# Optimization experiments

Measured on AMD Instinct MI355X. Metric: run time of the kernel, lower is better.

Reference implementation:

```python
import jax, jax.numpy as jnp
import numpy as np

# Fixed production-scale dims (see shape_source)
B, R, WIDTH, T, H, W = 8, 12, 2304, 4, 16, 29
REDUCE, HID, NC, ROI_SP, DEPTH = 1024, 512, 60, 7, 2
SR = 2  # roi_align sampling ratio (fixed; torchvision default -1 is roi-adaptive)


def conv2d(x, w, pad):
    return jax.lax.conv_general_dilated(
        x, w, (1, 1), [(pad, pad), (pad, pad)],
        dimension_numbers=('NCHW', 'OIHW', 'NCHW'))


def maxpool_3x3_s2(x):
    return jax.lax.reduce_window(
        x, -jnp.inf, jax.lax.max, (1, 1, 3, 3), (1, 1, 2, 2),
        [(0, 0), (0, 0), (1, 1), (1, 1)])


def bilinear(img, ys, xs):
    # img [C,h,w]; ys, xs [P] -> [C,P]; matches torchvision bilinear_interpolate
    h, w = img.shape[1], img.shape[2]
    valid = (ys >= -1.0) & (ys <= h) & (xs >= -1.0) & (xs <= w)
    y = jnp.clip(ys, 0.0, h - 1.0)
    x = jnp.clip(xs, 0.0, w - 1.0)
    y0f = jnp.floor(y); x0f = jnp.floor(x)
    iy0 = y0f.astype(jnp.int32); ix0 = x0f.astype(jnp.int32)
    iy1 = jnp.minimum(iy0 + 1, h - 1); ix1 = jnp.minimum(ix0 + 1, w - 1)
    ly = y - y0f; lx = x - x0f; hy = 1.0 - ly; hx = 1.0 - lx
    v00 = img[:, iy0, ix0]; v01 = img[:, iy0, ix1]
    v10 = img[:, iy1, ix0]; v11 = img[:, iy1, ix1]
    out = hy * hx * v00 + hy * lx * v01 + ly * hx * v10 + ly * lx * v11
    return jnp.where(valid[None, :], out, 0.0)


def roi_align_one(img, box):
    # img [C,H,W]; box (x1,y1,x2,y2) in feature coords; aligned=False, scale=1
    x1, y1, x2, y2 = box[0], box[1], box[2], box[3]
    rw = jnp.maximum(x2 - x1, 1.0)
    rh = jnp.maximum(y2 - y1, 1.0)
    bw = rw / ROI_SP; bh = rh / ROI_SP
    g = (jnp.arange(ROI_SP, dtype=jnp.float32)[:, None]
         + (jnp.arange(SR, dtype=jnp.float32)[None, :] + 0.5) / SR).reshape(-1)  # [7*SR]
    ys = y1 + g * bh; xs = x1 + g * bw
    n = ROI_SP * SR
    yy = jnp.repeat(ys, n); xx = jnp.tile(xs, n)
    vals = bilinear(img, yy, xx)                       # [C, n*n]
    vals = vals.reshape(img.shape[0], ROI_SP, SR, ROI_SP, SR)
    return vals.mean(axis=(2, 4))                      # [C,7,7]


def hr2o_layer(x, qw, kw, vw, cw, gamma, beta):
    # x [R, HID, Hp, Wp]; non-local attention across ROIs of one image
    q = conv2d(x, qw, 1)
    k = conv2d(x, kw, 1)
    v = conv2d(x, vw, 1)
    att = jnp.einsum('ichw,jchw->ijhw', q, k) / jnp.sqrt(jnp.float32(HID))
    att = jax.nn.softmax(att, axis=1)                  # softmax over key rois
    virt = jnp.einsum('ijhw,jchw->ichw', att, v)
    mu = virt.mean(axis=(1, 2, 3), keepdims=True)      # GroupNorm(1, HID)
    var = virt.var(axis=(1, 2, 3), keepdims=True)
    virt = (virt - mu) / jnp.sqrt(var + 1e-5)
    virt = virt * gamma[None, :, None, None] + beta[None, :, None, None]
    virt = jax.nn.relu(virt)
    virt = conv2d(virt, cw, 1)                         # mlp_1x1=False -> 3x3 pad 1
    return x + virt                                    # dropout inactive in eval


def setup_inputs() -> dict:
    key = jax.random.key(0)
    ks = jax.random.split(key, 14)
    features = jax.random.normal(ks[0], (B, WIDTH, T, H, W), jnp.float32)
    xy = jax.random.uniform(ks[1], (B, R, 2), minval=0.0, maxval=0.6)
    wh = jax.random.uniform(ks[2], (B, R, 2), minval=0.2, maxval=0.4)
    rois = jnp.concatenate([xy, xy + wh], axis=-1)     # normalized x1,y1,x2,y2

    def w_(k, shape, fan_in):
        return jax.random.normal(k, shape, jnp.float32) * (1.0 / np.sqrt(fan_in))

    return {
        'features': features,
        'rois': rois,
        'conv_reduce_w': w_(ks[3], (REDUCE, WIDTH, 1, 1), WIDTH),
        'conv1_w': w_(ks[4], (HID, 2 * REDUCE, 1, 1), 2 * REDUCE),
        'conv2_w': w_(ks[5], (HID, HID, 3, 3), HID * 9),
        'hr2o_qw': w_(ks[6], (DEPTH, HID, HID, 3, 3), HID * 9),
        'hr2o_kw': w_(ks[7], (DEPTH, HID, HID, 3, 3), HID * 9),
        'hr2o_vw': w_(ks[8], (DEPTH, HID, HID, 3, 3), HID * 9),
        'hr2o_cw': w_(ks[9], (DEPTH, HID, HID, 3, 3), HID * 9),
        'hr2o_gamma': jnp.ones((DEPTH, HID), jnp.float32),
        'hr2o_beta': jnp.zeros((DEPTH, HID), jnp.float32),
        'fc1_w': w_(ks[10], (HID, REDUCE), REDUCE),
        'fc2_w': w_(ks[11], (NC, 2 * HID), 2 * HID),
    }


def reference(features, rois, conv_reduce_w, conv1_w, conv2_w,
              hr2o_qw, hr2o_kw, hr2o_vw, hr2o_cw, hr2o_gamma, hr2o_beta,
              fc1_w, fc2_w):
    feats = features.mean(axis=2)                      # AdaptiveAvgPool3d((1,H,W)) over T
    feats = conv2d(feats, conv_reduce_w, 0)            # [B, REDUCE, H, W]

    scale = jnp.array([W, H, W, H], jnp.float32)
    boxes = rois * scale                               # feature-space coords (detached)
    ra = jax.vmap(lambda img, bxs: jax.vmap(lambda b: roi_align_one(img, b))(bxs))(
        feats, boxes)                                  # [B, R, REDUCE, 7, 7]
    roi_feats = ra.max(axis=(-2, -1)).reshape(B * R, REDUCE)  # MaxPool2d(7)

    # broadcast bg + tiled actor, concat on channels (eff_h=H, eff_w=W)
    bg = jnp.broadcast_to(feats[:, None], (B, R, REDUCE, H, W))
    actor = jnp.broadcast_to(
        roi_feats.reshape(B, R, REDUCE)[..., None, None], (B, R, REDUCE, H, W))
    x = jnp.concatenate([bg, actor], axis=2).reshape(B * R, 2 * REDUCE, H, W)
    x = jax.nn.relu(conv2d(x, conv1_w, 0))             # 1x1
    x = jax.nn.relu(conv2d(x, conv2_w, 0))             # 3x3, Conv2d default pad=0
    x = maxpool_3x3_s2(x)                              # [B*R, HID, 7, 14]
    hp, wp = x.shape[2], x.shape[3]
    x = x.reshape(B, R, HID, hp, wp)
    for d in range(DEPTH):
        x = jax.vmap(lambda xi: hr2o_layer(
            xi, hr2o_qw[d], hr2o_kw[d], hr2o_vw[d], hr2o_cw[d],
            hr2o_gamma[d], hr2o_beta[d]))(x)
    high = x.mean(axis=(-2, -1)).reshape(B * R, HID)   # GAP

    out = jax.nn.relu(roi_feats @ fc1_w.T)
    out = jnp.concatenate([out, high], axis=1)
    return out @ fc2_w.T                               # [B*R, NC]
```

## Files before the change

### kernel.cpp

```cpp
#include <hip/hip_runtime.h>
#include <math.h>

#define BB 8
#define RR 12
#define WIDTH 2304
#define TT 4
#define HH 16
#define WW 29
#define HWIN (HH*WW)
#define REDUCE 1024
#define HID 512
#define NC 60
#define DEPTH 2
#define NIMG (BB*RR)
#define OH2 14
#define OW2 27
#define NSP2 (OH2*OW2)
#define PH 7
#define PW 14
#define NSP (PH*PW)
#define ATT_SCALE 0.044194173824159216f

typedef __attribute__((ext_vector_type(8))) short short8;
typedef __attribute__((ext_vector_type(4))) float floatx4;

__device__ __forceinline__ void split2(float v, unsigned short& h, unsigned short& l)
{
    union { float f; unsigned u; } c; c.f = v;
    unsigned hb = c.u & 0xffff0000u;
    h = (unsigned short)(hb >> 16);
    union { float f; unsigned u; } hc; hc.u = hb;
    float r = v - hc.f;
    union { float f; unsigned u; } rc; rc.f = r;
    unsigned ru = rc.u + 0x7fffu + ((rc.u >> 16) & 1u);
    l = (unsigned short)(ru >> 16);
}

__device__ __forceinline__ void gll16(const void* g, void* l)
{
    __builtin_amdgcn_global_load_lds((const __attribute__((address_space(1))) void*)g,
                                     (__attribute__((address_space(3))) void*)l,
                                     16, 0, 0);
}

#define MFMA3(d, ah_, al_, bh_, bl_) \
    d = __builtin_amdgcn_mfma_f32_16x16x32_bf16(ah_, bh_, d, 0, 0, 0); \
    d = __builtin_amdgcn_mfma_f32_16x16x32_bf16(ah_, bl_, d, 0, 0, 0); \
    d = __builtin_amdgcn_mfma_f32_16x16x32_bf16(al_, bh_, d, 0, 0, 0);

template<int TYPE, int NSEL, bool RELU, bool RESID, int KW, int KSTN, int MTOT, long PLSTR, int NREAL>
__global__ __launch_bounds__(256, 2)
void tap2_k(const int4* __restrict__ WA0, const int4* __restrict__ WA1, const int4* __restrict__ WA2,
            const ushort* __restrict__ BH, const ushort* __restrict__ BL,
            const float* __restrict__ Res,
            float* __restrict__ Y0, float* __restrict__ Y1, float* __restrict__ Y2)
{
    __shared__ int4 L[3872];
    const int tid = threadIdx.x;
    const int z = blockIdx.z, nb = blockIdx.x;
    int by = blockIdx.y;

    const int4* WA = WA0; float* Y = Y0;
    if (NSEL == 3) {
        int sel = by >> 2; by &= 3;
        if (sel == 1) { WA = WA1; Y = Y1; }
        else if (sel == 2) { WA = WA2; Y = Y2; }
    }
    const int m0 = by * 128;
    const int lane = tid & 63, wv = tid >> 6;
    const int lrow = lane >> 4, lcol = lane & 15;
    constexpr long ALO = (long)KSTN * 4 * MTOT;

    int nU[2], gU[2]; long pbU[2]; bool vU[2];
#pragma unroll
    for (int it = 0; it < 2; ++it) {
        int u = tid + (it << 8);
        vU[it] = (u < 448);
        int uu = vU[it] ? u : 0;
        nU[it] = uu % 112; gU[it] = uu / 112;
        if (TYPE == 0) pbU[it] = nU[it];
        else {
            int gn = nb * 112 + nU[it];
            if (TYPE == 1) pbU[it] = (gn >> 5) * 29 + (gn & 31);
            else pbU[it] = min(gn, NREAL - 1);
        }
    }
    const ushort* BHz = BH + (size_t)z * PLSTR;
    const ushort* BLz = BL + (size_t)z * PLSTR;

    floatx4 acc[2][7];
#pragma unroll
    for (int mf = 0; mf < 2; ++mf)
#pragma unroll
        for (int nf = 0; nf < 7; ++nf) acc[mf][nf] = (floatx4){0.f, 0.f, 0.f, 0.f};

    short8 rbh[2], rbl[2];

#define STAGE_ISSUE(KST, BUF) { \
    int k8 = (KST) * 4; \
    _Pragma("unroll") \
    for (int j = 0; j < 4; ++j) { \
        int h = wv * 4 + j, p = h >> 3, g = (h >> 1) & 3, hf = h & 1; \
        gll16(WA + (p ? ALO : 0) + (long)(k8 + g) * MTOT + m0 + hf * 64 + lane, \
              L + (BUF) * 1936 + (p * 4 + g) * 129 + hf * 64); \
    } \
    int tap, ci0, shv; \
    if (TYPE == 2) { tap = 0; ci0 = (KST) << 5; shv = 0; } \
    else { tap = (KST) >> 4; ci0 = ((KST) & 15) << 5; int t3 = tap / 3; \
           shv = (TYPE == 0) ? t3 * 16 + (tap - t3 * 3) : t3 * 29 + (tap - t3 * 3); } \
    _Pragma("unroll") \
    for (int it = 0; it < 2; ++it) if (vU[it]) { \
        size_t o = (size_t)(pbU[it] + shv) * KW + ci0 + gU[it] * 8; \
        rbh[it] = *(const short8*)(BHz + o); \
        rbl[it] = *(const short8*)(BLz + o); \
    } }

#define STAGE_WRITE(BUF) { \
    _Pragma("unroll") \
    for (int it = 0; it < 2; ++it) if (vU[it]) { \
        *((short8*)(L + (BUF) * 1936 + 1032 + gU[it] * 113 + nU[it])) = rbh[it]; \
        *((short8*)(L + (BUF) * 1936 + 1484 + gU[it] * 113 + nU[it])) = rbl[it]; \
    } }

#define COMPUTE(BUF) { \
    const int4* Lc = L + (BUF) * 1936; \
    short8 ah[2], al[2]; \
    _Pragma("unroll") \
    for (int mf = 0; mf < 2; ++mf) { \
        int au = lrow * 129 + (wv * 2 + mf) * 16 + lcol; \
        ah[mf] = *(const short8*)(Lc + au); \
        al[mf] = *(const short8*)(Lc + 516 + au); \
    } \
    _Pragma("unroll") \
    for (int nf = 0; nf < 7; ++nf) { \
        int bu = 1032 + lrow * 113 + nf * 16 + lcol; \
        short8 bh = *(const short8*)(Lc + bu); \
        short8 bl = *(const short8*)(Lc + bu + 452); \
        _Pragma("unroll") \
        for (int mf = 0; mf < 2; ++mf) { MFMA3(acc[mf][nf], ah[mf], al[mf], bh, bl) } \
    } }

    STAGE_ISSUE(0, 0)
    STAGE_WRITE(0)
    __syncthreads();

    int cur = 0;
    for (int kst = 0; kst < KSTN; ++kst) {
        int nxt = cur ^ 1;
        bool more = (kst + 1 < KSTN);
        if (more) STAGE_ISSUE(kst + 1, nxt)
        COMPUTE(cur)
        if (more) { STAGE_WRITE(nxt) __syncthreads(); }
        cur = nxt;
    }

#pragma unroll
    for (int mf = 0; mf < 2; ++mf) {
        int m = m0 + wv * 32 + mf * 16 + lrow * 4;
#pragma unroll
        for (int nf = 0; nf < 7; ++nf) {
            int col = nf * 16 + lcol;
            int sp, realn; bool ok;
            if (TYPE == 0) { int oh = col >> 4, ow = col & 15; ok = ow < 14; sp = oh * 14 + ow; realn = 98; }
            else if (TYPE == 1) { int gn = nb * 112 + col; int oh = gn >> 5, ow = gn & 31; ok = ow < 27; sp = oh * 27 + ow; realn = 378; }
            else { int gn = nb * 112 + col; ok = gn < NREAL; sp = gn; realn = NREAL; }
            if (ok) {
#pragma unroll
                for (int r = 0; r < 4; ++r) {
                    size_t idx = ((size_t)z * MTOT + m + r) * realn + sp;
                    float v = acc[mf][nf][r];
                    if (RESID) v += Res[idx];
                    if (RELU) v = fmaxf(v, 0.f);
                    Y[idx] = v;
                }
            }
        }
    }
#undef STAGE_ISSUE
#undef STAGE_WRITE
#undef COMPUTE
}

__global__ void prep_w_k(const float* __restrict__ s0, const float* __restrict__ s1,
                         const float* __restrict__ s2, const float* __restrict__ s3,
                         int4* __restrict__ dst)
{
    const int c = blockIdx.y;
    const float* src = (c == 0) ? s0 : (c == 1) ? s1 : (c == 2) ? s2 : s3;
    int4* dh = dst + (size_t)c * 589824;
    int4* dl = dh + 294912;
    int idx = blockIdx.x * 256 + threadIdx.x;
    if (idx >= 294912) return;
    int g8 = idx / 512, m = idx & 511;
    unsigned hw[4], lw[4];
#pragma unroll
    for (int j = 0; j < 4; ++j) {
        int k1 = g8 * 8 + 2 * j, k2 = k1 + 1;
        float v1 = src[(size_t)m * 4608 + ((k1 & 511) * 9 + (k1 >> 9))];
        float v2 = src[(size_t)m * 4608 + ((k2 & 511) * 9 + (k2 >> 9))];
        unsigned short h0, l0, h1, l1;
        split2(v1, h0, l0); split2(v2, h1, l1);
        hw[j] = (unsigned)h0 | ((unsigned)h1 << 16);
        lw[j] = (unsigned)l0 | ((unsigned)l1 << 16);
    }
    dh[idx] = make_int4(hw[0], hw[1], hw[2], hw[3]);
    dl[idx] = make_int4(lw[0], lw[1], lw[2], lw[3]);
}

__global__ void prep_wg_k(const float* __restrict__ src, int ldw, int M, int K8,
                          int4* __restrict__ dst)
{
    int idx = blockIdx.x * 256 + threadIdx.x;
    if (idx >= K8 * M) return;
    int g8 = idx / M, m = idx % M;
    unsigned hw[4], lw[4];
#pragma unroll
    for (int j = 0; j < 4; ++j) {
        int k1 = g8 * 8 + 2 * j;
        float v1 = src[(size_t)m * ldw + k1];
        float v2 = src[(size_t)m * ldw + k1 + 1];
        unsigned short h0, l0, h1, l1;
        split2(v1, h0, l0); split2(v2, h1, l1);
        hw[j] = (unsigned)h0 | ((unsigned)h1 << 16);
        lw[j] = (unsigned)l0 | ((unsigned)l1 << 16);
    }
    dst[idx] = make_int4(hw[0], hw[1], hw[2], hw[3]);
    dst[(size_t)K8 * M + idx] = make_int4(lw[0], lw[1], lw[2], lw[3]);
}

__global__ __launch_bounds__(256)
void tsplit_k(const float* __restrict__ src, ushort* __restrict__ dh, ushort* __restrict__ dl,
              int C, int S, long zsrc, long zdst)
{
    __shared__ float t[64][65];
    const int c0 = blockIdx.x * 64, s0 = blockIdx.y * 64, z = blockIdx.z;
    const float* sz = src + (size_t)z * zsrc;
    const int tx = threadIdx.x & 63, ty = threadIdx.x >> 6;
#pragma unroll
    for (int i = 0; i < 16; ++i) {
        int cc = i * 4 + ty;
        int c = c0 + cc, s = s0 + tx;
        t[cc][tx] = (c < C && s < S) ? sz[(size_t)c * S + s] : 0.f;
    }
    __syncthreads();
#pragma unroll
    for (int i = 0; i < 16; ++i) {
        int ss = i * 4 + ty;
        int s = s0 + ss, c = c0 + tx;
        if (s < S && c < C) {
            unsigned short h, l;
            split2(t[tx][ss], h, l);
            size_t o = (size_t)z * zdst + (size_t)s * C + c;
            dh[o] = h; dl[o] = l;
        }
    }
}

__global__ __launch_bounds__(256)
void tsplit_c2_k(const float* __restrict__ bg, const float* __restrict__ bias1,
                 ushort* __restrict__ dh, ushort* __restrict__ dl)
{
    __shared__ float t[64][65];
    const int c0 = blockIdx.x * 64, s0 = blockIdx.y * 64, z = blockIdx.z;
    const int b = z / RR;
    const int tx = threadIdx.x & 63, ty = threadIdx.x >> 6;
#pragma unroll
    for (int i = 0; i < 16; ++i) {
        int cc = i * 4 + ty;
        int s = s0 + tx;
        t[cc][tx] = (s < 464) ? bg[((size_t)b * 512 + c0 + cc) * 464 + s] : 0.f;
    }
    __syncthreads();
    const float bv = bias1[z * 512 + c0 + tx];
#pragma unroll
    for (int i = 0; i < 16; ++i) {
        int ss = i * 4 + ty;
        int s = s0 + ss, c = c0 + tx;
        if (s < 472) {
            float v = (s < 464) ? fmaxf(t[tx][ss] + bv, 0.f) : 0.f;
            unsigned short h, l;
            split2(v, h, l);
            size_t o = (size_t)z * 241664 + (size_t)s * 512 + c;
            dh[o] = h; dl[o] = l;
        }
    }
}

__global__ __launch_bounds__(256)
void tsplit_pad_k(const float* __restrict__ x, ushort* __restrict__ dh, ushort* __restrict__ dl)
{
    __shared__ float t[64 * 99];
    const int c0 = blockIdx.x * 64, z = blockIdx.y;
    const int tid = threadIdx.x;
#pragma unroll
    for (int i = 0; i < 25; ++i) {
        int idx = tid + i * 256;
        if (idx < 6272) {
            int c = idx / 98, s = idx % 98;
            t[c * 99 + s] = x[((size_t)z * 512 + c0 + c) * 98 + s];
        }
    }
    __syncthreads();
#pragma unroll
    for (int i = 0; i < 40; ++i) {
        int idx = tid + i * 256;
        int sp = idx >> 6, c = idx & 63;
        int r = sp >> 4, col = sp & 15;
        float v = (r >= 1 && r <= 7 && col >= 1 && col <= 14) ? t[c * 99 + (r - 1) * 14 + col - 1] : 0.f;
        unsigned short h, l;
        split2(v, h, l);
        size_t o = (size_t)z * 81920 + (size_t)sp * 512 + c0 + c;
        dh[o] = h; dl[o] = l;
    }
}

__global__ void tmean_k(const float* __restrict__ f, float* __restrict__ o, int total)
{
    int i = blockIdx.x * blockDim.x + threadIdx.x;
    if (i >= total) return;
    int p = i % HWIN; long bc = i / HWIN;
    const float* src = f + bc * (long)TT * HWIN + p;
    o[i] = (src[0] + src[HWIN] + src[2 * HWIN] + src[3 * HWIN]) * 0.25f;
}

__global__ __launch_bounds__(256)
void roi_align_k(const float* __restrict__ feats, const float* __restrict__ rois,
                 float* __restrict__ roi_feats)
{
    __shared__ int s_o00[196], s_o01[196], s_o10[196], s_o11[196];
    __shared__ float s_w[4][196];
    const int n = blockIdx.x;
    const int b = n / RR;
    const int t = threadIdx.x;
    if (t < 196) {
        float x1 = rois[n * 4 + 0] * WW, y1 = rois[n * 4 + 1] * HH;
        float x2 = rois[n * 4 + 2] * WW, y2 = rois[n * 4 + 3] * HH;
        float rw = fmaxf(x2 - x1, 1.f), rh = fmaxf(y2 - y1, 1.f);
        float bw = rw / 7.f, bh = rh / 7.f;
        int j = t / 14, i = t % 14;
        float gy = (float)(j >> 1) + ((j & 1) + 0.5f) * 0.5f;
        float gx = (float)(i >> 1) + ((i & 1) + 0.5f) * 0.5f;
        float ys = y1 + gy * bh, xs = x1 + gx * bw;
        bool valid = (ys >= -1.f) && (ys <= (float)HH) && (xs >= -1.f) && (xs <= (float)WW);
        float y = fminf(fmaxf(ys, 0.f), (float)(HH - 1));
        float x = fminf(fmaxf(xs, 0.f), (float)(WW - 1));
        float y0f = floorf(y), x0f = floorf(x);
        int iy0 = (int)y0f, ix0 = (int)x0f;
        int iy1 = min(iy0 + 1, HH - 1), ix1 = min(ix0 + 1, WW - 1);
        float ly = y - y0f, lx = x - x0f, hy = 1.f - ly, hx = 1.f - lx;
        float msk = valid ? 1.f : 0.f;
        s_o00[t] = iy0 * WW + ix0; s_o01[t] = iy0 * WW + ix1;
        s_o10[t] = iy1 * WW + ix0; s_o11[t] = iy1 * WW + ix1;
        s_w[0][t] = hy * hx * msk; s_w[1][t] = hy * lx * msk;
        s_w[2][t] = ly * hx * msk; s_w[3][t] = ly * lx * msk;
    }
    __syncthreads();
    for (int c = t; c < REDUCE; c += 256) {
        const float* img = feats + ((long)(b * REDUCE + c)) * HWIN;
        float mx = -INFINITY;
        for (int bin = 0; bin < 49; ++bin) {
            int by_ = bin / 7, bx = bin % 7;
            float s = 0.f;
#pragma unroll
            for (int sy = 0; sy < 2; ++sy)
#pragma unroll
                for (int sx = 0; sx < 2; ++sx) {
                    int ss = (by_ * 2 + sy) * 14 + bx * 2 + sx;
                    s += s_w[0][ss] * img[s_o00[ss]] + s_w[1][ss] * img[s_o01[ss]]
                       + s_w[2][ss] * img[s_o10[ss]] + s_w[3][ss] * img[s_o11[ss]];
                }
            mx = fmaxf(mx, s * 0.25f);
        }
        roi_feats[(long)n * REDUCE + c] = mx;
    }
}

__global__ void dots_k(const float* __restrict__ Xr, const float* __restrict__ Wt,
                       int ldw, int woff, float* __restrict__ Y,
                       int Nrows, int M, int K, int relu)
{
    int idx = blockIdx.x * blockDim.x + threadIdx.x;
    if (idx >= Nrows * M) return;
    int o = idx / Nrows, n = idx % Nrows;
    const float* xr = Xr + (long)n * K;
    const float* w = Wt + (long)o * ldw + woff;
    float acc = 0.f;
    for (int k = 0; k < K; ++k) acc = fmaf(xr[k], w[k], acc);
    if (relu) acc = fmaxf(acc, 0.f);
    Y[(long)n * M + o] = acc;
}

__global__ void maxpool_k(const float* __restrict__ in, float* __restrict__ out, int total)
{
    int idx = blockIdx.x * blockDim.x + threadIdx.x;
    if (idx >= total) return;
    int ow = idx % PW; int r = idx / PW; int oh = r % PH; long nc = r / PH;
    const float* src = in + nc * NSP2;
    float m = -INFINITY;
    for (int kh = 0; kh < 3; ++kh) {
        int ih = oh * 2 - 1 + kh; if (ih < 0 || ih >= OH2) continue;
        for (int kw = 0; kw < 3; ++kw) {
            int iw = ow * 2 - 1 + kw; if (iw < 0 || iw >= OW2) continue;
            m = fmaxf(m, src[ih * OW2 + iw]);
        }
    }
    out[idx] = m;
}

__global__ void att_k(const float* __restrict__ q, const float* __restrict__ k,
                      float* __restrict__ att)
{
    int idx = blockIdx.x * blockDim.x + threadIdx.x;
    const int TOT = BB * 144 * 49;
    if (idx >= TOT) return;
    int ph = idx % 49; int r = idx / 49; int ij = r % 144; int b = r / 144;
    int i = ij / 12, j = ij % 12;
    int p = ph * 2;
    const float* qp = q + ((long)(b * RR + i) * HID) * NSP + p;
    const float* kp = k + ((long)(b * RR + j) * HID) * NSP + p;
    float a0 = 0.f, a1 = 0.f;
#pragma unroll 8
    for (int c = 0; c < HID; ++c) {
        float2 q2 = *(const float2*)(qp + (long)c * NSP);
        float2 k2 = *(const float2*)(kp + (long)c * NSP);
        a0 = fmaf(q2.x, k2.x, a0);
        a1 = fmaf(q2.y, k2.y, a1);
    }
    float* op = att + (((long)(b * 12 + i)) * 12 + j) * NSP + p;
    op[0] = a0 * ATT_SCALE;
    op[1] = a1 * ATT_SCALE;
}

__global__ void softmax_k(float* __restrict__ att)
{
    int idx = blockIdx.x * blockDim.x + threadIdx.x;
    const int TOT = BB * 12 * NSP;
    if (idx >= TOT) return;
    int p = idx % NSP; int r = idx / NSP; int i = r % 12; int b = r / 12;
    float* base = att + ((long)(b * 12 + i) * 12) * NSP + p;
    float v[12]; float m = -INFINITY;
#pragma unroll
    for (int j = 0; j < 12; ++j) { v[j] = base[j * NSP]; m = fmaxf(m, v[j]); }
    float s = 0.f;
#pragma unroll
    for (int j = 0; j < 12; ++j) { v[j] = expf(v[j] - m); s += v[j]; }
    float inv = 1.f / s;
#pragma unroll
    for (int j = 0; j < 12; ++j) base[j * NSP] = v[j] * inv;
}

__global__ void virt_k(const float* __restrict__ att, const float* __restrict__ v,
                       float* __restrict__ virt)
{
    int idx = blockIdx.x * blockDim.x + threadIdx.x;
    const int TOT = BB * RR * HID * 49;
    if (idx >= TOT) return;
    int ph = idx % 49; int r = idx / 49; int c = r % HID; int r2 = r / HID;
    int i = r2 % RR; int b = r2 / RR;
    int p = 2 * ph;
    const float* ap = att + ((long)(b * 12 + i) * 12) * NSP + p;
    float a0 = 0.f, a1 = 0.f;
#pragma unroll
    for (int j = 0; j < 12; ++j) {
        float w0 = ap[j * NSP], w1 = ap[j * NSP + 1];
        float2 v2 = *(const float2*)(v + (((long)(b * RR + j) * HID) + c) * NSP + p);
        a0 = fmaf(w0, v2.x, a0);
        a1 = fmaf(w1, v2.y, a1);
    }
    float* op = virt + (((long)(b * RR + i) * HID) + c) * NSP + p;
    op[0] = a0; op[1] = a1;
}

__global__ __launch_bounds__(256)
void stats_k(const float* __restrict__ virt, float* __restrict__ mu, float* __restrict__ rstd)
{
    int n = blockIdx.x;
    const float* src = virt + (long)n * HID * NSP;
    float s = 0.f, q = 0.f;
    for (int i = threadIdx.x; i < HID * NSP; i += 256) {
        float v = src[i]; s += v; q = fmaf(v, v, q);
    }
    for (int off = 32; off; off >>= 1) { s += __shfl_down(s, off); q += __shfl_down(q, off); }
    __shared__ float ss[4], sq[4];
    int w = threadIdx.x >> 6;
    if ((threadIdx.x & 63) == 0) { ss[w] = s; sq[w] = q; }
    __syncthreads();
    if (threadIdx.x == 0) {
        float S = ss[0] + ss[1] + ss[2] + ss[3];
        float Q = sq[0] + sq[1] + sq[2] + sq[3];
        const float invN = 1.f / (HID * NSP);
        float m = S * invN;
        float var = Q * invN - m * m;
        mu[n] = m; rstd[n] = rsqrtf(var + 1e-5f);
    }
}

__global__ void norm_k(float* __restrict__ virt, const float* __restrict__ mu,
                       const float* __restrict__ rstd,
                       const float* __restrict__ gamma, const float* __restrict__ beta)
{
    int idx = blockIdx.x * blockDim.x + threadIdx.x;
    const int TOT = NIMG * HID * NSP;
    if (idx >= TOT) return;
    int n = idx / (HID * NSP);
    int c = (idx / NSP) % HID;
    float val = (virt[idx] - mu[n]) * rstd[n] * gamma[c] + beta[c];
    virt[idx] = fmaxf(val, 0.f);
}

__global__ void meanpool_k(const float* __restrict__ x, float* __restrict__ high)
{
    int idx = blockIdx.x * blockDim.x + threadIdx.x;
    if (idx >= NIMG * HID) return;
    const float* src = x + (long)idx * NSP;
    float s = 0.f;
    for (int p = 0; p < NSP; ++p) s += src[p];
    high[idx] = s * (1.f / NSP);
}

__global__ void final_k(const float* __restrict__ fc1o, const float* __restrict__ high,
                        const float* __restrict__ fc2, float* __restrict__ out)
{
    int idx = blockIdx.x * blockDim.x + threadIdx.x;
    if (idx >= NIMG * NC) return;
    int n = idx / NC, o = idx % NC;
    const float* w = fc2 + (long)o * (2 * HID);
    const float* a = fc1o + (long)n * HID;
    const float* h = high + (long)n * HID;
    float acc = 0.f;
    for (int c = 0; c < HID; ++c) acc = fmaf(a[c], w[c], acc);
    for (int c = 0; c < HID; ++c) acc = fmaf(h[c], w[HID + c], acc);
    out[idx] = acc;
}

extern "C" void kernel_launch(void* const* d_in, const int* in_sizes, int n_in,
                              void* d_out, int out_size, void* d_ws, size_t ws_size,
                              hipStream_t stream)
{
    (void)in_sizes; (void)n_in; (void)out_size; (void)ws_size;
    const float* features = (const float*)d_in[0];
    const float* rois     = (const float*)d_in[1];
    const float* w_reduce = (const float*)d_in[2];
    const float* w_conv1  = (const float*)d_in[3];
    const float* w_conv2  = (const float*)d_in[4];
    const float* qw       = (const float*)d_in[5];
    const float* kw       = (const float*)d_in[6];
    const float* vw       = (const float*)d_in[7];
    const float* cw       = (const float*)d_in[8];
    const float* gamma    = (const float*)d_in[9];
    const float* beta     = (const float*)d_in[10];
    const float* fc1      = (const float*)d_in[11];
    const float* fc2      = (const float*)d_in[12];
    float* ws = (float*)d_ws;

    float*  tmean = ws + 0;
    ushort* tmTH  = (ushort*)(ws + 8552448);
    ushort* tmTL  = (ushort*)(ws + 12828672);
    float*  feats = ws + 17104896;
    ushort* ftTH  = (ushort*)(ws + 0);
    ushort* ftTL  = (ushort*)(ws + 1900544);
    ushort* B2H   = (ushort*)(ws + 0);
    ushort* B2L   = (ushort*)(ws + 11599872);
    int4*   WTQ   = (int4*)(ws + 0);
    float*  bg    = ws + 23199744;
    float*  out2  = ws + 23199744;
    float*  qb    = ws + 23199744;
    float*  kb    = ws + 28016640;
    float*  vb    = ws + 32833536;
    ushort* PTH   = (ushort*)(ws + 41779200);
    ushort* PTL   = (ushort*)(ws + 45711360);
    float*  xb    = ws + 49643520;
    float*  virt  = ws + 54460416;
    int4*   WTS   = (int4*)(ws + 59277312);
    float*  rf    = ws + 61636608;
    float*  bias1 = ws + 61734912;
    float*  fc1o  = ws + 61784064;
    float*  attb  = ws + 61833216;
    float*  mu    = ws + 61946112;
    float*  rstd  = ws + 61946240;
    float*  high  = ws + 61946368;

    dim3 blk(256);

    prep_wg_k<<<1152, blk, 0, stream>>>(w_reduce, 2304, 1024, 288, WTS);

    { int tot = BB * WIDTH * HWIN;
      tmean_k<<<(tot + 255) / 256, blk, 0, stream>>>(features, tmean, tot); }

    tsplit_k<<<dim3(36, 8, 8), blk, 0, stream>>>(tmean, tmTH, tmTL, 2304, 464, 1069056, 1069056);

    tap2_k<2, 1, false, false, 2304, 72, 1024, 464L * 2304, 464>
        <<<dim3(5, 8, 8), blk, 0, stream>>>(WTS, nullptr, nullptr, tmTH, tmTL, nullptr,
                                            feats, nullptr, nullptr);

    tsplit_k<<<dim3(16, 8, 8), blk, 0, stream>>>(feats, ftTH, ftTL, 1024, 464, 475136, 475136);

    roi_align_k<<<96, blk, 0, stream>>>(feats, rois, rf);
    dots_k<<<(NIMG * HID + 255) / 256, blk, 0, stream>>>(rf, w_conv1, 2048, 1024, bias1, NIMG, HID, REDUCE, 0);
    dots_k<<<(NIMG * HID + 255) / 256, blk, 0, stream>>>(rf, fc1, 1024, 0, fc1o, NIMG, HID, REDUCE, 1);

    prep_wg_k<<<256, blk, 0, stream>>>(w_conv1, 2048, 512, 128, WTS);
    tap2_k<2, 1, false, false, 1024, 32, 512, 464L * 1024, 464>
        <<<dim3(5, 4, 8), blk, 0, stream>>>(WTS, nullptr, nullptr, ftTH, ftTL, nullptr,
                                            bg, nullptr, nullptr);

    prep_w_k<<<dim3(1152, 1), blk, 0, stream>>>(w_conv2, w_conv2, w_conv2, w_conv2, WTS);
    tsplit_c2_k<<<dim3(8, 8, 96), blk, 0, stream>>>(bg, bias1, B2H, B2L);

    tap2_k<1, 1, true, false, 512, 144, 512, 472L * 512, 378>
        <<<dim3(4, 4, 96), blk, 0, stream>>>(WTS, nullptr, nullptr, B2H, B2L, nullptr,
                                             out2, nullptr, nullptr);

    { int tot = NIMG * HID * NSP;
      maxpool_k<<<(tot + 255) / 256, blk, 0, stream>>>(out2, xb, tot); }

    for (int d = 0; d < DEPTH; ++d) {
        long woff = (long)d * HID * HID * 9;
        prep_w_k<<<dim3(1152, 4), blk, 0, stream>>>(qw + woff, kw + woff, vw + woff, cw + woff, WTQ);

        tsplit_pad_k<<<dim3(8, 96), blk, 0, stream>>>(xb, PTH, PTL);
        tap2_k<0, 3, false, false, 512, 144, 512, 160L * 512, 98>
            <<<dim3(1, 12, 96), blk, 0, stream>>>(WTQ, WTQ + 589824, WTQ + 2 * 589824,
                                                  PTH, PTL, nullptr, qb, kb, vb);

        { int tot = BB * 144 * 49;
          att_k<<<(tot + 255) / 256, blk, 0, stream>>>(qb, kb, attb); }
        { int tot = BB * 12 * NSP;
          softmax_k<<<(tot + 255) / 256, blk, 0, stream>>>(attb); }
        { int tot = BB * RR * HID * 49;
          virt_k<<<(tot + 255) / 256, blk, 0, stream>>>(attb, vb, virt); }
        stats_k<<<96, blk, 0, stream>>>(virt, mu, rstd);
        { int tot = NIMG * HID * NSP;
          norm_k<<<(tot + 255) / 256, blk, 0, stream>>>(virt, mu, rstd, gamma + d * HID, beta + d * HID); }

        tsplit_pad_k<<<dim3(8, 96), blk, 0, stream>>>(virt, PTH, PTL);
        tap2_k<0, 1, false, true, 512, 144, 512, 160L * 512, 98>
            <<<dim3(1, 4, 96), blk, 0, stream>>>(WTQ + 3 * 589824, nullptr, nullptr,
                                                 PTH, PTL, xb, xb, nullptr, nullptr);
    }

    meanpool_k<<<(NIMG * HID + 255) / 256, blk, 0, stream>>>(xb, high);
    final_k<<<(NIMG * NC + 255) / 256, blk, 0, stream>>>(fc1o, high, fc2, (float*)d_out);
}
```

Measured before the change: 3.405 ms.

## Fuse attention scores with softmax, tile via LDS, and reorder conv grid dims

Replaces the separate attention-score, softmax and weighted-sum kernels with two LDS-tiled kernels. The first stages q/k chunks in shared memory and applies the softmax in-block. The second caches the whole per-image attention matrix in shared memory and reuses each v load across all 12 output ROIs. The 3x3 conv launches also swap the grid so the image index runs on blockIdx.x, which changes block scheduling order and weight reuse across concurrently running blocks. The new attention kernels launch very few blocks (112 and 64), which risks under-filling the GPU.

```diff
diff --git a/kernel.cpp b/kernel.cpp
--- a/kernel.cpp
+++ b/kernel.cpp
@@ -48,7 +48,7 @@
     d = __builtin_amdgcn_mfma_f32_16x16x32_bf16(ah_, bl_, d, 0, 0, 0); \
     d = __builtin_amdgcn_mfma_f32_16x16x32_bf16(al_, bh_, d, 0, 0, 0);
 
-template<int TYPE, int NSEL, bool RELU, bool RESID, int KW, int KSTN, int MTOT, long PLSTR, int NREAL>
+template<int TYPE, int NSEL, bool RELU, bool RESID, int KW, int KSTN, int MTOT, long PLSTR, int NREAL, bool ZX>
 __global__ __launch_bounds__(256, 2)
 void tap2_k(const int4* __restrict__ WA0, const int4* __restrict__ WA1, const int4* __restrict__ WA2,
             const ushort* __restrict__ BH, const ushort* __restrict__ BL,
@@ -57,7 +57,8 @@
 {
     __shared__ int4 L[3872];
     const int tid = threadIdx.x;
-    const int z = blockIdx.z, nb = blockIdx.x;
+    const int z  = ZX ? blockIdx.x : blockIdx.z;
+    const int nb = ZX ? blockIdx.z : blockIdx.x;
     int by = blockIdx.y;
 
     const int4* WA = WA0; float* Y = Y0;
@@ -407,68 +408,91 @@
     out[idx] = m;
 }
 
-__global__ void att_k(const float* __restrict__ q, const float* __restrict__ k,
-                      float* __restrict__ att)
-{
-    int idx = blockIdx.x * blockDim.x + threadIdx.x;
-    const int TOT = BB * 144 * 49;
-    if (idx >= TOT) return;
-    int ph = idx % 49; int r = idx / 49; int ij = r % 144; int b = r / 144;
-    int i = ij / 12, j = ij % 12;
-    int p = ph * 2;
-    const float* qp = q + ((long)(b * RR + i) * HID) * NSP + p;
-    const float* kp = k + ((long)(b * RR + j) * HID) * NSP + p;
-    float a0 = 0.f, a1 = 0.f;
+__global__ __launch_bounds__(256)
+void att2_k(const float* __restrict__ q, const float* __restrict__ k, float* __restrict__ att)
+{
+    __shared__ float qs[5376];
+    __shared__ float ks[5376];
+    __shared__ float sc[1008];
+    const int b = blockIdx.x, p0 = blockIdx.y * 7;
+    const int tid = threadIdx.x;
+
+    int itI[4], itJ[4], itP[4]; bool itV[4];
+#pragma unroll
+    for (int r = 0; r < 4; ++r) {
+        int item = tid + (r << 8);
+        itV[r] = item < 1008;
+        int it = itV[r] ? item : 0;
+        int ij = it / 7; itP[r] = it % 7;
+        itI[r] = ij / 12; itJ[r] = ij % 12;
+    }
+    float acc[4] = {0.f, 0.f, 0.f, 0.f};
+
+    for (int cc0 = 0; cc0 < 512; cc0 += 64) {
+        for (int l = tid; l < 5376; l += 256) {
+            int i = l / 448, r = l % 448, c = r / 7, p = r % 7;
+            size_t off = ((size_t)(b * 12 + i) * 512 + cc0 + c) * 98 + p0 + p;
+            qs[l] = q[off];
+            ks[l] = k[off];
+        }
+        __syncthreads();
+#pragma unroll
+        for (int r = 0; r < 4; ++r) {
+            if (itV[r]) {
+                const float* qp = qs + itI[r] * 448 + itP[r];
+                const float* kp = ks + itJ[r] * 448 + itP[r];
+                float a = acc[r];
 #pragma unroll 8
-    for (int c = 0; c < HID; ++c) {
-        float2 q2 = *(const float2*)(qp + (long)c * NSP);
-        float2 k2 = *(const float2*)(kp + (long)c * NSP);
-        a0 = fmaf(q2.x, k2.x, a0);
-        a1 = fmaf(q2.y, k2.y, a1);
-    }
-    float* op = att + (((long)(b * 12 + i)) * 12 + j) * NSP + p;
-    op[0] = a0 * ATT_SCALE;
-    op[1] = a1 * ATT_SCALE;
-}
-
-__global__ void softmax_k(float* __restrict__ att)
-{
-    int idx = blockIdx.x * blockDim.x + threadIdx.x;
-    const int TOT = BB * 12 * NSP;
-    if (idx >= TOT) return;
-    int p = idx % NSP; int r = idx / NSP; int i = r % 12; int b = r / 12;
-    float* base = att + ((long)(b * 12 + i) * 12) * NSP + p;
-    float v[12]; float m = -INFINITY;
-#pragma unroll
-    for (int j = 0; j < 12; ++j) { v[j] = base[j * NSP]; m = fmaxf(m, v[j]); }
-    float s = 0.f;
-#pragma unroll
-    for (int j = 0; j < 12; ++j) { v[j] = expf(v[j] - m); s += v[j]; }
-    float inv = 1.f / s;
-#pragma unroll
-    for (int j = 0; j < 12; ++j) base[j * NSP] = v[j] * inv;
-}
-
-__global__ void virt_k(const float* __restrict__ att, const float* __restrict__ v,
-                       float* __restrict__ virt)
-{
-    int idx = blockIdx.x * blockDim.x + threadIdx.x;
-    const int TOT = BB * RR * HID * 49;
-    if (idx >= TOT) return;
-    int ph = idx % 49; int r = idx / 49; int c = r % HID; int r2 = r / HID;
-    int i = r2 % RR; int b = r2 / RR;
-    int p = 2 * ph;
-    const float* ap = att + ((long)(b * 12 + i) * 12) * NSP + p;
-    float a0 = 0.f, a1 = 0.f;
-#pragma unroll
-    for (int j = 0; j < 12; ++j) {
-        float w0 = ap[j * NSP], w1 = ap[j * NSP + 1];
-        float2 v2 = *(const float2*)(v + (((long)(b * RR + j) * HID) + c) * NSP + p);
-        a0 = fmaf(w0, v2.x, a0);
-        a1 = fmaf(w1, v2.y, a1);
-    }
-    float* op = virt + (((long)(b * RR + i) * HID) + c) * NSP + p;
-    op[0] = a0; op[1] = a1;
+                for (int c = 0; c < 64; ++c) a = fmaf(qp[c * 7], kp[c * 7], a);
+                acc[r] = a;
+            }
+        }
+        __syncthreads();
+    }
+#pragma unroll
+    for (int r = 0; r < 4; ++r)
+        if (itV[r]) sc[tid + (r << 8)] = acc[r] * ATT_SCALE;
+    __syncthreads();
+    if (tid < 84) {
+        int i = tid / 7, p = tid % 7;
+        float m = -INFINITY;
+        float v[12];
+#pragma unroll
+        for (int j = 0; j < 12; ++j) { v[j] = sc[(i * 12 + j) * 7 + p]; m = fmaxf(m, v[j]); }
+        float s = 0.f;
+#pragma unroll
+        for (int j = 0; j < 12; ++j) { v[j] = expf(v[j] - m); s += v[j]; }
+        float inv = 1.f / s;
+#pragma unroll
+        for (int j = 0; j < 12; ++j)
+            att[((size_t)(b * 12 + i) * 12 + j) * 98 + p0 + p] = v[j] * inv;
+    }
+}
+
+__global__ __launch_bounds__(256)
+void virt2_k(const float* __restrict__ att, const float* __restrict__ v, float* __restrict__ virt)
+{
+    __shared__ float as_[14112];
+    const int b = blockIdx.x, cb = blockIdx.y;
+    const int tid = threadIdx.x;
+    for (int l = tid; l < 14112; l += 256) as_[l] = att[(size_t)b * 14112 + l];
+    __syncthreads();
+
+    for (int it = tid; it < 6272; it += 256) {
+        int c = cb * 64 + it / 98, p = it % 98;
+        float o[12];
+#pragma unroll
+        for (int i = 0; i < 12; ++i) o[i] = 0.f;
+#pragma unroll
+        for (int j = 0; j < 12; ++j) {
+            float vj = v[((size_t)(b * 12 + j) * 512 + c) * 98 + p];
+#pragma unroll
+            for (int i = 0; i < 12; ++i) o[i] = fmaf(as_[(i * 12 + j) * 98 + p], vj, o[i]);
+        }
+#pragma unroll
+        for (int i = 0; i < 12; ++i)
+            virt[((size_t)(b * 12 + i) * 512 + c) * 98 + p] = o[i];
+    }
 }
 
 __global__ __launch_bounds__(256)
@@ -589,7 +613,7 @@
 
     tsplit_k<<<dim3(36, 8, 8), blk, 0, stream>>>(tmean, tmTH, tmTL, 2304, 464, 1069056, 1069056);
 
-    tap2_k<2, 1, false, false, 2304, 72, 1024, 464L * 2304, 464>
+    tap2_k<2, 1, false, false, 2304, 72, 1024, 464L * 2304, 464, false>
         <<<dim3(5, 8, 8), blk, 0, stream>>>(WTS, nullptr, nullptr, tmTH, tmTL, nullptr,
                                             feats, nullptr, nullptr);
 
@@ -600,15 +624,15 @@
     dots_k<<<(NIMG * HID + 255) / 256, blk, 0, stream>>>(rf, fc1, 1024, 0, fc1o, NIMG, HID, REDUCE, 1);
 
     prep_wg_k<<<256, blk, 0, stream>>>(w_conv1, 2048, 512, 128, WTS);
-    tap2_k<2, 1, false, false, 1024, 32, 512, 464L * 1024, 464>
+    tap2_k<2, 1, false, false, 1024, 32, 512, 464L * 1024, 464, false>
         <<<dim3(5, 4, 8), blk, 0, stream>>>(WTS, nullptr, nullptr, ftTH, ftTL, nullptr,
                                             bg, nullptr, nullptr);
 
     prep_w_k<<<dim3(1152, 1), blk, 0, stream>>>(w_conv2, w_conv2, w_conv2, w_conv2, WTS);
     tsplit_c2_k<<<dim3(8, 8, 96), blk, 0, stream>>>(bg, bias1, B2H, B2L);
 
-    tap2_k<1, 1, true, false, 512, 144, 512, 472L * 512, 378>
-        <<<dim3(4, 4, 96), blk, 0, stream>>>(WTS, nullptr, nullptr, B2H, B2L, nullptr,
+    tap2_k<1, 1, true, false, 512, 144, 512, 472L * 512, 378, true>
+        <<<dim3(96, 4, 4), blk, 0, stream>>>(WTS, nullptr, nullptr, B2H, B2L, nullptr,
                                              out2, nullptr, nullptr);
 
     { int tot = NIMG * HID * NSP;
@@ -619,23 +643,19 @@
         prep_w_k<<<dim3(1152, 4), blk, 0, stream>>>(qw + woff, kw + woff, vw + woff, cw + woff, WTQ);
 
         tsplit_pad_k<<<dim3(8, 96), blk, 0, stream>>>(xb, PTH, PTL);
-        tap2_k<0, 3, false, false, 512, 144, 512, 160L * 512, 98>
-            <<<dim3(1, 12, 96), blk, 0, stream>>>(WTQ, WTQ + 589824, WTQ + 2 * 589824,
+        tap2_k<0, 3, false, false, 512, 144, 512, 160L * 512, 98, true>
+            <<<dim3(96, 12, 1), blk, 0, stream>>>(WTQ, WTQ + 589824, WTQ + 2 * 589824,
                                                   PTH, PTL, nullptr, qb, kb, vb);
 
-        { int tot = BB * 144 * 49;
-          att_k<<<(tot + 255) / 256, blk, 0, stream>>>(qb, kb, attb); }
-        { int tot = BB * 12 * NSP;
-          softmax_k<<<(tot + 255) / 256, blk, 0, stream>>>(attb); }
-        { int tot = BB * RR * HID * 49;
-          virt_k<<<(tot + 255) / 256, blk, 0, stream>>>(attb, vb, virt); }
+        att2_k<<<dim3(8, 14), blk, 0, stream>>>(qb, kb, attb);
+        virt2_k<<<dim3(8, 8), blk, 0, stream>>>(attb, vb, virt);
         stats_k<<<96, blk, 0, stream>>>(virt, mu, rstd);
         { int tot = NIMG * HID * NSP;
           norm_k<<<(tot + 255) / 256, blk, 0, stream>>>(virt, mu, rstd, gamma + d * HID, beta + d * HID); }
 
         tsplit_pad_k<<<dim3(8, 96), blk, 0, stream>>>(virt, PTH, PTL);
-        tap2_k<0, 1, false, true, 512, 144, 512, 160L * 512, 98>
-            <<<dim3(1, 4, 96), blk, 0, stream>>>(WTQ + 3 * 589824, nullptr, nullptr,
+        tap2_k<0, 1, false, true, 512, 144, 512, 160L * 512, 98, true>
+            <<<dim3(96, 4, 1), blk, 0, stream>>>(WTQ + 3 * 589824, nullptr, nullptr,
                                                  PTH, PTL, xb, xb, nullptr, nullptr);
     }
 
```

After: 3.314 ms. 1.03x faster.
